# Kernel tuning notes

Hardware: AMD Instinct MI355X
Metric: run time of the kernel (lower is better)

Reference implementation:

```python
import jax, jax.numpy as jnp
import numpy as np

B, M, N, E = 64, 100, 6400, 102400   # graphs, nodes/graph, total nodes, edges
H, D, EMB, IMG, NC = 4, 512, 768, 1024, 2
HD = H * D
EPS = 1e-5


def _bn2(x, g, b, m, v):
    # BatchNorm1d eval mode on [B, C]
    return (x - m) / jnp.sqrt(v + EPS) * g + b


def _bn3(x, g, b, m, v):
    # BatchNorm1d eval mode on [B, C, L] -> channel dim is axis 1 (node index)
    return (x - m[None, :, None]) / jnp.sqrt(v + EPS)[None, :, None] * g[None, :, None] + b[None, :, None]


def _gat(feat, src, dst, W, al, ar, bias):
    # DGL GATConv (eval: feat_drop is identity). feat: [N, F_in]
    h = (feat @ W.T).reshape(-1, H, D)                 # [N, H, D]
    el = (h * al[None]).sum(-1)                         # [N, H]
    er = (h * ar[None]).sum(-1)                         # [N, H]
    e = jax.nn.leaky_relu(el[src] + er[dst], negative_slope=0.2)  # [E, H]
    mx = jax.ops.segment_max(e, dst, num_segments=N)
    a = jnp.exp(e - mx[dst])
    s = jax.ops.segment_sum(a, dst, num_segments=N)
    alpha = a / s[dst]                                  # edge softmax over incoming edges
    out = jax.ops.segment_sum(h[src] * alpha[:, :, None], dst, num_segments=N)  # [N, H, D]
    return out + bias.reshape(1, H, D)


def setup_inputs() -> dict:
    key = jax.random.key(0)
    ks = iter(jax.random.split(key, 80))
    n = lambda *s: jax.random.normal(next(ks), s, dtype=jnp.float32)

    def bn(c):
        return (1.0 + 0.1 * n(c), 0.1 * n(c), 0.1 * n(c),
                0.5 + jax.random.uniform(next(ks), (c,), dtype=jnp.float32))

    s = 0.02
    inp = {}
    inp['img_embedding'] = n(B, IMG)
    inp['func_text_embedding'] = n(B, EMB)
    inp['unix_emb'] = n(N, EMB)
    inp['pos_emb'] = jax.random.uniform(next(ks), (N, 4), dtype=jnp.float32)
    inp['src'] = jax.random.randint(next(ks), (E,), 0, N)
    inp['dst'] = jax.random.randint(next(ks), (E,), 0, N)
    inp['gat1_W'] = n(HD, EMB) * s; inp['gat1_al'] = n(H, D) * 0.1; inp['gat1_ar'] = n(H, D) * 0.1; inp['gat1_b'] = jnp.zeros(HD)
    inp['gat2_W'] = n(HD, HD) * s; inp['gat2_al'] = n(H, D) * 0.1; inp['gat2_ar'] = n(H, D) * 0.1; inp['gat2_b'] = jnp.zeros(HD)
    inp['fc_W'] = n(D, HD) * s; inp['fc_b'] = jnp.zeros(D)
    inp['hidden_W'] = n(8, D, D) * s; inp['hidden_b'] = jnp.zeros((8, D))
    inp['bn_text_g'], inp['bn_text_b'], inp['bn_text_m'], inp['bn_text_v'] = bn(EMB)
    inp['fc_text_W'] = n(D, EMB) * s; inp['fc_text_b'] = jnp.zeros(D)
    inp['swin_g'], inp['swin_b'], inp['swin_m'], inp['swin_v'] = bn(IMG)
    inp['swinfc_W'] = n(D, IMG) * s; inp['swinfc_b'] = jnp.zeros(D)
    inp['bngat_g'], inp['bngat_b'], inp['bngat_m'], inp['bngat_v'] = bn(M)
    inp['fc_gat_W'] = n(480, D) * s; inp['fc_gat_b'] = jnp.zeros(480)
    inp['bnbb_g'], inp['bnbb_b'], inp['bnbb_m'], inp['bnbb_v'] = bn(M)
    inp['fc_bbox_W'] = n(32, 4) * s; inp['fc_bbox_b'] = jnp.zeros(32)
    inp['fbn_g'], inp['fbn_b'], inp['fbn_m'], inp['fbn_v'] = bn(3 * D)
    inp['final_W'] = n(NC, 3 * D) * s; inp['final_b'] = jnp.zeros(NC)
    return inp


def reference(img_embedding, func_text_embedding, unix_emb, pos_emb, src, dst,
              gat1_W, gat1_al, gat1_ar, gat1_b, gat2_W, gat2_al, gat2_ar, gat2_b,
              fc_W, fc_b, hidden_W, hidden_b,
              bn_text_g, bn_text_b, bn_text_m, bn_text_v, fc_text_W, fc_text_b,
              swin_g, swin_b, swin_m, swin_v, swinfc_W, swinfc_b,
              bngat_g, bngat_b, bngat_m, bngat_v, fc_gat_W, fc_gat_b,
              bnbb_g, bnbb_b, bnbb_m, bnbb_v, fc_bbox_W, fc_bbox_b,
              fbn_g, fbn_b, fbn_m, fbn_v, final_W, final_b):
    # image branch
    x = jax.nn.elu(_bn2(img_embedding, swin_g, swin_b, swin_m, swin_v) @ swinfc_W.T + swinfc_b)
    # text branch
    ft = jax.nn.elu(_bn2(func_text_embedding, bn_text_g, bn_text_b, bn_text_m, bn_text_v) @ fc_text_W.T + fc_text_b)
    # graph branch: two stacked GATConv layers (dropout is identity in eval)
    h = _gat(unix_emb, src, dst, gat1_W, gat1_al, gat1_ar, gat1_b).reshape(N, HD)
    h = _gat(h, src, dst, gat2_W, gat2_al, gat2_ar, gat2_b).reshape(N, HD)
    h = jax.nn.elu(h @ fc_W.T + fc_b)
    for i in range(8):
        h = jax.nn.elu(h @ hidden_W[i].T + hidden_b[i])
    # unbatch + pad to max_node=100 -> pure reshape (all graphs have exactly M nodes)
    h_i = h.reshape(B, M, D)
    pos_i = pos_emb.reshape(B, M, 4)
    h_i = jax.nn.elu(_bn3(h_i, bngat_g, bngat_b, bngat_m, bngat_v) @ fc_gat_W.T + fc_gat_b)      # [B, M, 480]
    pos_i = jax.nn.elu(_bn3(pos_i, bnbb_g, bnbb_b, bnbb_m, bnbb_v) @ fc_bbox_W.T + fc_bbox_b)    # [B, M, 32]
    h_feature = jnp.concatenate([h_i, pos_i], axis=2).mean(axis=1)                                # [B, 512]
    all_feats = jnp.concatenate([x, h_feature, ft], axis=1)                                       # [B, 1536]
    return _bn2(all_feats, fbn_g, fbn_b, fbn_m, fbn_v) @ final_W.T + final_b
```

## Files before the change

kernel.cpp:

```cpp
#include <hip/hip_runtime.h>
#include <math.h>

#define Bg   64
#define Mg   100
#define Ng   6400
#define Eg   102400
#define Hh   4
#define Dd   512
#define HDd  2048
#define EMBd 768
#define IMGd 1024
#define EPSc 1e-5f

typedef __bf16 bf16x8 __attribute__((ext_vector_type(8)));
typedef float  f32x4  __attribute__((ext_vector_type(4)));

#define SBAR __builtin_amdgcn_sched_barrier(0)
#define WBAR __builtin_amdgcn_s_barrier()

__device__ __forceinline__ float eluf(float x) { return x > 0.f ? x : expm1f(x); }

__device__ __forceinline__ unsigned short f2bf(float x) {
    unsigned int u = __builtin_bit_cast(unsigned int, x);
    u += 0x7FFFu + ((u >> 16) & 1u);
    return (unsigned short)(u >> 16);
}
__device__ __forceinline__ float bf2f(unsigned short s) {
    return __builtin_bit_cast(float, ((unsigned int)s) << 16);
}

__device__ __forceinline__ void gld16(const void* g, void* l) {
    __builtin_amdgcn_global_load_lds(
        (const __attribute__((address_space(1))) void*)g,
        (__attribute__((address_space(3))) void*)l, 16, 0, 0);
}

__global__ __launch_bounds__(512, 2)
void gemm_bf16_256(const unsigned short* __restrict__ A,
                   const unsigned short* __restrict__ W,
                   const float* __restrict__ bias, void* __restrict__ C,
                   int M, int N, int K, int act, int outbf)
{
    __shared__ __align__(16) unsigned short As[2][256 * 64];
    __shared__ __align__(16) unsigned short Bs[2][256 * 64];

    const int tid  = threadIdx.x;
    const int lane = tid & 63, wid = tid >> 6;
    const int wm = wid >> 2, wn = wid & 3;
    const int bm = blockIdx.y * 256, bn = blockIdx.x * 256;
    const int fl = lane & 15;
    const int fsl = lane >> 4;

    f32x4 acc[8][4] = {};
    bf16x8 a_[4][2];
    bf16x8 b_[2][2][2];

    const int NT = K >> 6;

    const int srow0 = tid >> 3;
    const int scol  = (((tid & 7) ^ ((tid >> 3) & 7)) << 3);
    const unsigned short* pAs = A + (size_t)(bm + srow0) * K + scol;
    const unsigned short* pBs = W + (size_t)(bn + srow0) * K + scol;
    const size_t K64 = (size_t)K * 64, K128 = (size_t)K * 128;

#define STGA(kt, h, d)                                                        \
    do {                                                                      \
        gld16(pAs + (h) * K128 + ((kt) << 6),                                 \
              (char*)As[d] + (h) * 16384 + wid * 1024);                       \
        gld16(pAs + (h) * K128 + K64 + ((kt) << 6),                           \
              (char*)As[d] + (h) * 16384 + 8192 + wid * 1024);                \
    } while (0)
#define STGB(kt, h, d)                                                        \
    do {                                                                      \
        gld16(pBs + (h) * K128 + ((kt) << 6),                                 \
              (char*)Bs[d] + (h) * 16384 + wid * 1024);                       \
        gld16(pBs + (h) * K128 + K64 + ((kt) << 6),                           \
              (char*)Bs[d] + (h) * 16384 + 8192 + wid * 1024);                \
    } while (0)

#define LDA(qm, d)                                                            \
    _Pragma("unroll") for (int i = 0; i < 4; ++i)                             \
    _Pragma("unroll") for (int kk = 0; kk < 2; ++kk) {                        \
        int r_  = wm * 128 + (qm) * 64 + i * 16 + fl;                         \
        int sl_ = ((kk << 2) + fsl) ^ (fl & 7);                               \
        a_[i][kk] = *(const bf16x8*)((const char*)As[d] + r_ * 128 + (sl_ << 4)); \
    }
#define LDB(qn, d)                                                            \
    _Pragma("unroll") for (int j = 0; j < 2; ++j)                             \
    _Pragma("unroll") for (int kk = 0; kk < 2; ++kk) {                        \
        int r_  = wn * 64 + (qn) * 32 + j * 16 + fl;                          \
        int sl_ = ((kk << 2) + fsl) ^ (fl & 7);                               \
        b_[qn][j][kk] = *(const bf16x8*)((const char*)Bs[d] + r_ * 128 + (sl_ << 4)); \
    }
#define PHMM(qm, qn)                                                          \
    do {                                                                      \
        WBAR;                                                                 \
        __builtin_amdgcn_s_setprio(1);                                        \
        _Pragma("unroll") for (int kk = 0; kk < 2; ++kk)                      \
        _Pragma("unroll") for (int i = 0; i < 4; ++i)                         \
        _Pragma("unroll") for (int j = 0; j < 2; ++j)                         \
            acc[(qm) * 4 + i][(qn) * 2 + j] =                                 \
                __builtin_amdgcn_mfma_f32_16x16x32_bf16(                      \
                    a_[i][kk], b_[qn][j][kk],                                 \
                    acc[(qm) * 4 + i][(qn) * 2 + j], 0, 0, 0);                \
        __builtin_amdgcn_s_setprio(0);                                        \
        WBAR;                                                                 \
    } while (0)

    STGB(0, 0, 0); STGB(0, 1, 0);
    STGA(0, 0, 0); STGA(0, 1, 0);
    STGB(1, 0, 1); STGB(1, 1, 1);
    asm volatile("s_waitcnt vmcnt(4)" ::: "memory");
    WBAR;

    for (int j = 0; j < (NT >> 1); ++j) {
        const int O = 2 * j + 1;
        const int g1 = (2 * j + 2 < NT), g2 = (2 * j + 3 < NT);

        LDA(0, 0); LDB(0, 0);
        STGA(O, 0, 1);
        PHMM(0, 0);

        LDB(1, 0);
        STGA(O, 1, 1);
        PHMM(0, 1);

        LDA(1, 0);
        if (g1) STGB(2 * j + 2, 0, 0);
        PHMM(1, 0);

        if (g1) STGB(2 * j + 2, 1, 0);
        if (g1) { asm volatile("s_waitcnt vmcnt(4)" ::: "memory"); }
        else    { asm volatile("s_waitcnt vmcnt(0)" ::: "memory"); }
        PHMM(1, 1);

        LDA(0, 1); LDB(0, 1);
        if (g1) STGA(2 * j + 2, 0, 0);
        PHMM(0, 0);

        LDB(1, 1);
        if (g1) STGA(2 * j + 2, 1, 0);
        PHMM(0, 1);

        LDA(1, 1);
        if (g2) STGB(2 * j + 3, 0, 1);
        PHMM(1, 0);

        if (g2) STGB(2 * j + 3, 1, 1);
        if (g1) { asm volatile("s_waitcnt vmcnt(4)" ::: "memory"); }
        else    { asm volatile("s_waitcnt vmcnt(0)" ::: "memory"); }
        PHMM(1, 1);
    }

#undef STGA
#undef STGB
#undef LDA
#undef LDB
#undef PHMM

    const int crow0 = bm + wm * 128 + ((lane >> 4) << 2);
    const int ccol0 = bn + wn * 64 + fl;
#pragma unroll
    for (int fr = 0; fr < 8; ++fr) {
#pragma unroll
        for (int fc = 0; fc < 4; ++fc) {
            int col = ccol0 + fc * 16;
            float bv = bias ? bias[col] : 0.f;
#pragma unroll
            for (int rr = 0; rr < 4; ++rr) {
                int row = crow0 + fr * 16 + rr;
                float v = acc[fr][fc][rr] + bv;
                if (act) v = eluf(v);
                if (outbf) ((unsigned short*)C)[(size_t)row * N + col] = f2bf(v);
                else       ((float*)C)[(size_t)row * N + col] = v;
            }
        }
    }
}

__global__ __launch_bounds__(256)
void gemm_bf16_t64(const unsigned short* __restrict__ A,
                   const unsigned short* __restrict__ W,
                   const float* __restrict__ bias, void* __restrict__ C,
                   int M, int N, int K, int act, int outbf)
{
    __shared__ __align__(16) unsigned short As[2][64 * 32];
    __shared__ __align__(16) unsigned short Bs[2][64 * 32];
    const int tid  = threadIdx.x;
    const int lane = tid & 63, wid = tid >> 6;
    const int bm = blockIdx.y * 64, bn = blockIdx.x * 64;
    const int wm = (wid >> 1) * 32, wn = (wid & 1) * 32;
    const int lrow = lane >> 2;
    const int lcol = (((lane & 3) ^ ((lane >> 3) & 3)) << 3);

    f32x4 acc[2][2] = {};

    const int ra = wid * 16;
    const unsigned short* gA = A + (size_t)(bm + ra + lrow) * K + lcol;
    int rb = bn + ra + lrow; if (rb >= N) rb = N - 1;
    const unsigned short* gB = W + (size_t)rb * K + lcol;

    const int frow = lane & 15;
    const int qsw = (((lane >> 4) ^ ((frow >> 1) & 3)) << 3);
    const int nt = K >> 5;

#define STAGE64(t, b)                           \
    do {                                        \
        const int k0_ = (t) << 5;               \
        gld16(gA + k0_, &As[b][ra * 32]);       \
        gld16(gB + k0_, &Bs[b][ra * 32]);       \
    } while (0)

    STAGE64(0, 0);
    if (nt > 1) STAGE64(1, 1);

    for (int t = 0; t < nt; ++t) {
        const int bi = t & 1;
        if (t + 1 < nt) { asm volatile("s_waitcnt vmcnt(2)" ::: "memory"); }
        else            { asm volatile("s_waitcnt vmcnt(0)" ::: "memory"); }
        WBAR;

        bf16x8 af0 = *(const bf16x8*)&As[bi][(wm + frow) * 32 + qsw];
        bf16x8 af1 = *(const bf16x8*)&As[bi][(wm + 16 + frow) * 32 + qsw];
        bf16x8 bf0 = *(const bf16x8*)&Bs[bi][(wn + frow) * 32 + qsw];
        bf16x8 bf1 = *(const bf16x8*)&Bs[bi][(wn + 16 + frow) * 32 + qsw];
        acc[0][0] = __builtin_amdgcn_mfma_f32_16x16x32_bf16(af0, bf0, acc[0][0], 0, 0, 0);
        acc[0][1] = __builtin_amdgcn_mfma_f32_16x16x32_bf16(af0, bf1, acc[0][1], 0, 0, 0);
        acc[1][0] = __builtin_amdgcn_mfma_f32_16x16x32_bf16(af1, bf0, acc[1][0], 0, 0, 0);
        acc[1][1] = __builtin_amdgcn_mfma_f32_16x16x32_bf16(af1, bf1, acc[1][1], 0, 0, 0);

        WBAR;
        if (t + 2 < nt) STAGE64(t + 2, bi);
    }
#undef STAGE64

    const int crow0 = bm + wm + ((lane >> 4) << 2);
    const int ccol0 = bn + wn + (lane & 15);
#pragma unroll
    for (int mi = 0; mi < 2; ++mi) {
#pragma unroll
        for (int ni = 0; ni < 2; ++ni) {
            int col = ccol0 + ni * 16;
            if (col >= N) continue;
            float bv = bias ? bias[col] : 0.f;
#pragma unroll
            for (int r = 0; r < 4; ++r) {
                int row = crow0 + mi * 16 + r;
                float v = acc[mi][ni][r] + bv;
                if (act) v = eluf(v);
                if (outbf) ((unsigned short*)C)[(size_t)row * N + col] = f2bf(v);
                else       ((float*)C)[(size_t)row * N + col] = v;
            }
        }
    }
}

__global__ __launch_bounds__(256)
void gemm_nt(const float* __restrict__ A, const float* __restrict__ W,
             const float* __restrict__ bias, float* __restrict__ C,
             int M, int N, int K, int act)
{
    __shared__ float As[16 * 68];
    __shared__ float Ws[16 * 68];
    const int tid = threadIdx.x;
    const int tx = tid & 15, ty = tid >> 4;
    const int bm = blockIdx.y * 64, bn = blockIdx.x * 64;
    const int lrow = tid >> 2;
    const int lk4  = (tid & 3) << 2;
    const int arow = bm + lrow;
    const int wrow = bn + lrow;
    const float* Aptr = A + (size_t)arow * K + lk4;
    const float* Wptr = W + (size_t)wrow * K + lk4;
    float acc[4][4] = {{0.f,0.f,0.f,0.f},{0.f,0.f,0.f,0.f},{0.f,0.f,0.f,0.f},{0.f,0.f,0.f,0.f}};

    for (int k0 = 0; k0 < K; k0 += 16) {
        float4 av = make_float4(0.f,0.f,0.f,0.f);
        float4 wv = make_float4(0.f,0.f,0.f,0.f);
        if (arow < M) av = *(const float4*)(Aptr + k0);
        if (wrow < N) wv = *(const float4*)(Wptr + k0);
        As[(lk4+0)*68 + lrow] = av.x;
        As[(lk4+1)*68 + lrow] = av.y;
        As[(lk4+2)*68 + lrow] = av.z;
        As[(lk4+3)*68 + lrow] = av.w;
        Ws[(lk4+0)*68 + lrow] = wv.x;
        Ws[(lk4+1)*68 + lrow] = wv.y;
        Ws[(lk4+2)*68 + lrow] = wv.z;
        Ws[(lk4+3)*68 + lrow] = wv.w;
        __syncthreads();
#pragma unroll
        for (int kk = 0; kk < 16; ++kk) {
            float4 a = *(const float4*)&As[kk*68 + (ty<<2)];
            float4 w = *(const float4*)&Ws[kk*68 + (tx<<2)];
            acc[0][0] += a.x*w.x; acc[0][1] += a.x*w.y; acc[0][2] += a.x*w.z; acc[0][3] += a.x*w.w;
            acc[1][0] += a.y*w.x; acc[1][1] += a.y*w.y; acc[1][2] += a.y*w.z; acc[1][3] += a.y*w.w;
            acc[2][0] += a.z*w.x; acc[2][1] += a.z*w.y; acc[2][2] += a.z*w.z; acc[2][3] += a.z*w.w;
            acc[3][0] += a.w*w.x; acc[3][1] += a.w*w.y; acc[3][2] += a.w*w.z; acc[3][3] += a.w*w.w;
        }
        __syncthreads();
    }

#pragma unroll
    for (int i = 0; i < 4; ++i) {
        int row = bm + (ty<<2) + i;
        int col = bn + (tx<<2);
        if (row < M && col < N) {
            float4 v;
            v.x = acc[i][0]; v.y = acc[i][1]; v.z = acc[i][2]; v.w = acc[i][3];
            if (bias) { v.x += bias[col]; v.y += bias[col+1]; v.z += bias[col+2]; v.w += bias[col+3]; }
            if (act == 1) { v.x = eluf(v.x); v.y = eluf(v.y); v.z = eluf(v.z); v.w = eluf(v.w); }
            *(float4*)(C + (size_t)row * N + col) = v;
        }
    }
}

struct CvtPack {
    const float* s[6];
    unsigned short* d[6];
    int n4[6];
};

__global__ void cvt_all(CvtPack p, int total4)
{
    int i = blockIdx.x * 256 + threadIdx.x;
    if (i >= total4) return;
#pragma unroll
    for (int k = 0; k < 6; ++k) {
        if (i < p.n4[k]) {
            float4 v = ((const float4*)p.s[k])[i];
            ushort4 o;
            o.x = f2bf(v.x); o.y = f2bf(v.y); o.z = f2bf(v.z); o.w = f2bf(v.w);
            ((ushort4*)p.d[k])[i] = o;
            return;
        }
        i -= p.n4[k];
    }
}

__global__ void bn_col(const float* __restrict__ x, const float* __restrict__ g,
                       const float* __restrict__ b, const float* __restrict__ m,
                       const float* __restrict__ v, float* __restrict__ y,
                       int rows, int cols)
{
    int i = blockIdx.x * 256 + threadIdx.x;
    if (i >= rows * cols) return;
    int c = i % cols;
    float inv = rsqrtf(v[c] + EPSc);
    y[i] = (x[i] - m[c]) * inv * g[c] + b[c];
}

__global__ void bn_node_b4(const ushort4* __restrict__ x, const float* __restrict__ g,
                           const float* __restrict__ b, const float* __restrict__ m,
                           const float* __restrict__ v, ushort4* __restrict__ y,
                           int total4, int Cdim4)
{
    int i = blockIdx.x * 256 + threadIdx.x;
    if (i >= total4) return;
    int n = i / Cdim4;
    int p = n % Mg;
    float sc = rsqrtf(v[p] + EPSc) * g[p];
    float sh = b[p] - m[p] * sc;
    ushort4 xv = x[i];
    ushort4 o;
    o.x = f2bf(bf2f(xv.x) * sc + sh);
    o.y = f2bf(bf2f(xv.y) * sc + sh);
    o.z = f2bf(bf2f(xv.z) * sc + sh);
    o.w = f2bf(bf2f(xv.w) * sc + sh);
    y[i] = o;
}

__global__ void zero_i32(int* __restrict__ p, int n)
{
    int i = blockIdx.x * 256 + threadIdx.x;
    if (i < n) p[i] = 0;
}

__global__ void count_dst(const int* __restrict__ dst, int* __restrict__ counts, int E)
{
    int i = blockIdx.x * 256 + threadIdx.x;
    if (i < E) atomicAdd(&counts[dst[i]], 1);
}

__global__ __launch_bounds__(1024)
void scan_excl(const int* __restrict__ counts, int* __restrict__ offs,
               int* __restrict__ cursor, int n)
{
    __shared__ int sm[1024];
    __shared__ int carry;
    if (threadIdx.x == 0) carry = 0;
    __syncthreads();
    for (int base = 0; base < n; base += 1024) {
        int i = base + (int)threadIdx.x;
        int v = (i < n) ? counts[i] : 0;
        sm[threadIdx.x] = v;
        __syncthreads();
        for (int o = 1; o < 1024; o <<= 1) {
            int t = (threadIdx.x >= (unsigned)o) ? sm[threadIdx.x - o] : 0;
            __syncthreads();
            sm[threadIdx.x] += t;
            __syncthreads();
        }
        int incl = sm[threadIdx.x];
        int myc = carry;
        if (i < n) {
            int ex = myc + incl - v;
            offs[i] = ex;
            cursor[i] = ex;
        }
        __syncthreads();
        if (threadIdx.x == 1023) carry = myc + sm[1023];
        __syncthreads();
    }
    if (threadIdx.x == 0) offs[n] = carry;
}

__global__ void scatter_edges(const int* __restrict__ dst, int* __restrict__ cursor,
                              int* __restrict__ eid, int E)
{
    int i = blockIdx.x * 256 + threadIdx.x;
    if (i < E) {
        int p = atomicAdd(&cursor[dst[i]], 1);
        eid[p] = i;
    }
}

__global__ __launch_bounds__(256)
void elr_kernel(const unsigned short* __restrict__ Hm, const float* __restrict__ al,
                const float* __restrict__ ar, float* __restrict__ el,
                float* __restrict__ er)
{
    int wid = threadIdx.x >> 6, lane = threadIdx.x & 63;
    int g = (blockIdx.x << 2) + wid;
    int n = g >> 2, h = g & 3;
    const unsigned short* hp = Hm + ((size_t)n << 11) + (h << 9) + (lane << 3);
    const float* alp = al + (h << 9) + (lane << 3);
    const float* arp = ar + (h << 9) + (lane << 3);
    ushort4 x0 = *(const ushort4*)hp;
    ushort4 x1 = *(const ushort4*)(hp + 4);
    float4 l0 = *(const float4*)alp, l1 = *(const float4*)(alp + 4);
    float4 r0 = *(const float4*)arp, r1 = *(const float4*)(arp + 4);
    float a0 = bf2f(x0.x), a1 = bf2f(x0.y), a2 = bf2f(x0.z), a3 = bf2f(x0.w);
    float a4 = bf2f(x1.x), a5 = bf2f(x1.y), a6 = bf2f(x1.z), a7 = bf2f(x1.w);
    float se = a0*l0.x + a1*l0.y + a2*l0.z + a3*l0.w + a4*l1.x + a5*l1.y + a6*l1.z + a7*l1.w;
    float sr = a0*r0.x + a1*r0.y + a2*r0.z + a3*r0.w + a4*r1.x + a5*r1.y + a6*r1.z + a7*r1.w;
#pragma unroll
    for (int o = 32; o > 0; o >>= 1) {
        se += __shfl_down(se, o, 64);
        sr += __shfl_down(sr, o, 64);
    }
    if (lane == 0) { el[g] = se; er[g] = sr; }
}

__global__ __launch_bounds__(256)
void gat_agg(const unsigned short* __restrict__ Hm, const float* __restrict__ el,
             const float* __restrict__ er, const int* __restrict__ src,
             const int* __restrict__ offs, const int* __restrict__ eid,
             const float* __restrict__ bias, unsigned short* __restrict__ out)
{
    int n = blockIdx.x;
    int tid = threadIdx.x;
    int beg = offs[n], end = offs[n + 1];
    int deg = end - beg;
    const int b0 = tid << 2;
    const int b1 = 1024 + (tid << 2);
    const int h0 = tid >> 7;
    const int h1 = h0 + 2;

    if (deg == 0) {
#pragma unroll
        for (int j = 0; j < 4; ++j) {
            out[((size_t)n << 11) + b0 + j] = f2bf(bias[b0 + j]);
            out[((size_t)n << 11) + b1 + j] = f2bf(bias[b1 + j]);
        }
        return;
    }

    __shared__ float m_sh[4], s_sh[4], al_sh[4];
    __shared__ int   src_sh[128];
    __shared__ float logit_sh[512];
    __shared__ float w_sh[512];

    if (tid < 4) { m_sh[tid] = -INFINITY; s_sh[tid] = 0.f; }
    float acc[8] = {0.f,0.f,0.f,0.f,0.f,0.f,0.f,0.f};
    __syncthreads();

    for (int c0 = 0; c0 < deg; c0 += 128) {
        int cnt = min(128, deg - c0);
        for (int i = tid; i < cnt; i += 256) src_sh[i] = src[eid[beg + c0 + i]];
        __syncthreads();
        for (int idx = tid; idx < (cnt << 2); idx += 256) {
            int i = idx >> 2, h = idx & 3;
            float x = el[(src_sh[i] << 2) + h] + er[(n << 2) + h];
            logit_sh[idx] = x > 0.f ? x : 0.2f * x;
        }
        __syncthreads();
        if (tid < 4) {
            float cm = -INFINITY;
            for (int i = 0; i < cnt; ++i) cm = fmaxf(cm, logit_sh[(i << 2) + tid]);
            float mn = fmaxf(m_sh[tid], cm);
            al_sh[tid] = expf(m_sh[tid] - mn);
            m_sh[tid] = mn;
        }
        __syncthreads();
        for (int idx = tid; idx < (cnt << 2); idx += 256)
            w_sh[idx] = expf(logit_sh[idx] - m_sh[idx & 3]);
        __syncthreads();
        if (tid < 4) {
            float cs = 0.f;
            for (int i = 0; i < cnt; ++i) cs += w_sh[(i << 2) + tid];
            s_sh[tid] = s_sh[tid] * al_sh[tid] + cs;
        }
        float r0 = al_sh[h0], r1 = al_sh[h1];
        acc[0] *= r0; acc[1] *= r0; acc[2] *= r0; acc[3] *= r0;
        acc[4] *= r1; acc[5] *= r1; acc[6] *= r1; acc[7] *= r1;
        for (int i = 0; i < cnt; ++i) {
            const unsigned short* hp = Hm + ((size_t)src_sh[i] << 11);
            ushort4 a = *(const ushort4*)(hp + b0);
            ushort4 b = *(const ushort4*)(hp + b1);
            float w0 = w_sh[(i << 2) + h0], w1 = w_sh[(i << 2) + h1];
            acc[0] += w0 * bf2f(a.x); acc[1] += w0 * bf2f(a.y);
            acc[2] += w0 * bf2f(a.z); acc[3] += w0 * bf2f(a.w);
            acc[4] += w1 * bf2f(b.x); acc[5] += w1 * bf2f(b.y);
            acc[6] += w1 * bf2f(b.z); acc[7] += w1 * bf2f(b.w);
        }
        __syncthreads();
    }

    float is0 = 1.f / s_sh[h0], is1 = 1.f / s_sh[h1];
#pragma unroll
    for (int j = 0; j < 4; ++j) {
        out[((size_t)n << 11) + b0 + j] = f2bf(acc[j] * is0 + bias[b0 + j]);
        out[((size_t)n << 11) + b1 + j] = f2bf(acc[4 + j] * is1 + bias[b1 + j]);
    }
}

__global__ void mean_kernel(const float* __restrict__ hg, const float* __restrict__ pos,
                            const float* __restrict__ bg, const float* __restrict__ bb_,
                            const float* __restrict__ bm_, const float* __restrict__ bv_,
                            const float* __restrict__ W, const float* __restrict__ bias,
                            float* __restrict__ hf)
{
    int i = blockIdx.x * 256 + threadIdx.x;
    if (i >= Bg * Dd) return;
    int bb = i >> 9, c = i & 511;
    float s = 0.f;
    if (c < 480) {
        const float* p = hg + (size_t)bb * Mg * 480 + c;
        for (int mm = 0; mm < Mg; ++mm) s += p[mm * 480];
    } else {
        int o = c - 480;
        float w0 = W[(o << 2) + 0], w1 = W[(o << 2) + 1];
        float w2 = W[(o << 2) + 2], w3 = W[(o << 2) + 3];
        float bo = bias[o];
        const float* pp = pos + (size_t)bb * Mg * 4;
        for (int mm = 0; mm < Mg; ++mm) {
            float sc = rsqrtf(bv_[mm] + EPSc) * bg[mm];
            float sh = bb_[mm] - bm_[mm] * sc;
            float a = bo + (pp[mm*4+0]*sc+sh)*w0 + (pp[mm*4+1]*sc+sh)*w1
                         + (pp[mm*4+2]*sc+sh)*w2 + (pp[mm*4+3]*sc+sh)*w3;
            s += eluf(a);
        }
    }
    hf[i] = s * 0.01f;
}

__global__ __launch_bounds__(256)
void final_kernel(const float* __restrict__ x, const float* __restrict__ hf,
                  const float* __restrict__ ft, const float* __restrict__ g,
                  const float* __restrict__ b, const float* __restrict__ m,
                  const float* __restrict__ v, const float* __restrict__ W,
                  const float* __restrict__ bias, float* __restrict__ out)
{
    int bb = blockIdx.x;
    int tid = threadIdx.x;
    float a0 = 0.f, a1 = 0.f;
    for (int c = tid; c < 1536; c += 256) {
        float xv = (c < 512) ? x[bb * 512 + c]
                 : (c < 1024) ? hf[bb * 512 + (c - 512)]
                              : ft[bb * 512 + (c - 1024)];
        float z = (xv - m[c]) * rsqrtf(v[c] + EPSc) * g[c] + b[c];
        a0 += z * W[c];
        a1 += z * W[1536 + c];
    }
    __shared__ float r0[256], r1[256];
    r0[tid] = a0; r1[tid] = a1;
    __syncthreads();
    for (int o = 128; o > 0; o >>= 1) {
        if (tid < o) { r0[tid] += r0[tid + o]; r1[tid] += r1[tid + o]; }
        __syncthreads();
    }
    if (tid == 0) {
        out[bb * 2 + 0] = r0[0] + bias[0];
        out[bb * 2 + 1] = r1[0] + bias[1];
    }
}

extern "C" void kernel_launch(void* const* d_in, const int* in_sizes, int n_in,
                              void* d_out, int out_size, void* d_ws, size_t ws_size,
                              hipStream_t stream)
{
    (void)in_sizes; (void)n_in; (void)out_size; (void)ws_size;

    const float* img   = (const float*)d_in[0];
    const float* ftxt  = (const float*)d_in[1];
    const float* unixe = (const float*)d_in[2];
    const float* pos   = (const float*)d_in[3];
    const int*   src   = (const int*)  d_in[4];
    const int*   dst   = (const int*)  d_in[5];
    const float* g1W   = (const float*)d_in[6];
    const float* g1al  = (const float*)d_in[7];
    const float* g1ar  = (const float*)d_in[8];
    const float* g1b   = (const float*)d_in[9];
    const float* g2W   = (const float*)d_in[10];
    const float* g2al  = (const float*)d_in[11];
    const float* g2ar  = (const float*)d_in[12];
    const float* g2b   = (const float*)d_in[13];
    const float* fcW   = (const float*)d_in[14];
    const float* fcb   = (const float*)d_in[15];
    const float* hidW  = (const float*)d_in[16];
    const float* hidb  = (const float*)d_in[17];
    const float* btg   = (const float*)d_in[18];
    const float* btb   = (const float*)d_in[19];
    const float* btm   = (const float*)d_in[20];
    const float* btv   = (const float*)d_in[21];
    const float* ftW   = (const float*)d_in[22];
    const float* ftbi  = (const float*)d_in[23];
    const float* swg   = (const float*)d_in[24];
    const float* swb   = (const float*)d_in[25];
    const float* swm   = (const float*)d_in[26];
    const float* swv   = (const float*)d_in[27];
    const float* swW   = (const float*)d_in[28];
    const float* swbi  = (const float*)d_in[29];
    const float* bgg   = (const float*)d_in[30];
    const float* bgb   = (const float*)d_in[31];
    const float* bgm   = (const float*)d_in[32];
    const float* bgv   = (const float*)d_in[33];
    const float* fgW   = (const float*)d_in[34];
    const float* fgb   = (const float*)d_in[35];
    const float* bbgp  = (const float*)d_in[36];
    const float* bbbp  = (const float*)d_in[37];
    const float* bbmp  = (const float*)d_in[38];
    const float* bbvp  = (const float*)d_in[39];
    const float* fbW   = (const float*)d_in[40];
    const float* fbb   = (const float*)d_in[41];
    const float* fng   = (const float*)d_in[42];
    const float* fnb   = (const float*)d_in[43];
    const float* fnm   = (const float*)d_in[44];
    const float* fnv   = (const float*)d_in[45];
    const float* fiW   = (const float*)d_in[46];
    const float* fib   = (const float*)d_in[47];
    float* out = (float*)d_out;

    char* p = (char*)d_ws;
    unsigned short* fA  = (unsigned short*)p; p += (size_t)Ng * HDd * 2;
    unsigned short* fB  = (unsigned short*)p; p += (size_t)Ng * HDd * 2;
    unsigned short* fC  = (unsigned short*)p; p += (size_t)Ng * Dd * 2;
    unsigned short* fD  = (unsigned short*)p; p += (size_t)Ng * Dd * 2;
    float*          fE  = (float*)p;          p += (size_t)Ng * 480 * 4;
    float*          el  = (float*)p;          p += (size_t)Ng * Hh * 4;
    float*          er  = (float*)p;          p += (size_t)Ng * Hh * 4;
    float*          xb  = (float*)p;          p += (size_t)Bg * Dd * 4;
    float*          ftb = (float*)p;          p += (size_t)Bg * Dd * 4;
    float*          hf  = (float*)p;          p += (size_t)Bg * Dd * 4;
    float*          ti  = (float*)p;          p += (size_t)Bg * IMGd * 4;
    float*          tt  = (float*)p;          p += (size_t)Bg * EMBd * 4;
    unsigned short* ubf = (unsigned short*)p; p += (size_t)Ng * EMBd * 2;
    unsigned short* wg1 = (unsigned short*)p; p += (size_t)HDd * EMBd * 2;
    unsigned short* wg2 = (unsigned short*)p; p += (size_t)HDd * HDd * 2;
    unsigned short* wfc = (unsigned short*)p; p += (size_t)Dd * HDd * 2;
    unsigned short* whid= (unsigned short*)p; p += (size_t)8 * Dd * Dd * 2;
    unsigned short* wfg = (unsigned short*)p; p += (size_t)480 * Dd * 2;
    int* counts = (int*)p; p += (size_t)Ng * 4;
    int* offs   = (int*)p; p += (size_t)(Ng + 1) * 4 + 12;
    int* cursor = (int*)p; p += (size_t)Ng * 4;
    int* eid    = (int*)p; p += (size_t)Eg * 4;

    CvtPack cp;
    cp.s[0] = unixe; cp.d[0] = ubf;  cp.n4[0] = Ng * EMBd / 4;
    cp.s[1] = g1W;   cp.d[1] = wg1;  cp.n4[1] = HDd * EMBd / 4;
    cp.s[2] = g2W;   cp.d[2] = wg2;  cp.n4[2] = HDd * HDd / 4;
    cp.s[3] = fcW;   cp.d[3] = wfc;  cp.n4[3] = Dd * HDd / 4;
    cp.s[4] = hidW;  cp.d[4] = whid; cp.n4[4] = 8 * Dd * Dd / 4;
    cp.s[5] = fgW;   cp.d[5] = wfg;  cp.n4[5] = 480 * Dd / 4;
    int total4 = cp.n4[0] + cp.n4[1] + cp.n4[2] + cp.n4[3] + cp.n4[4] + cp.n4[5];
    cvt_all<<<(total4 + 255)/256, 256, 0, stream>>>(cp, total4);

    bn_col<<<(Bg*IMGd + 255)/256, 256, 0, stream>>>(img, swg, swb, swm, swv, ti, Bg, IMGd);
    gemm_nt<<<dim3(8, 1), 256, 0, stream>>>(ti, swW, swbi, xb, Bg, Dd, IMGd, 1);
    bn_col<<<(Bg*EMBd + 255)/256, 256, 0, stream>>>(ftxt, btg, btb, btm, btv, tt, Bg, EMBd);
    gemm_nt<<<dim3(8, 1), 256, 0, stream>>>(tt, ftW, ftbi, ftb, Bg, Dd, EMBd, 1);

    zero_i32<<<(Ng + 255)/256, 256, 0, stream>>>(counts, Ng);
    count_dst<<<(Eg + 255)/256, 256, 0, stream>>>(dst, counts, Eg);
    scan_excl<<<1, 1024, 0, stream>>>(counts, offs, cursor, Ng);
    scatter_edges<<<(Eg + 255)/256, 256, 0, stream>>>(dst, cursor, eid, Eg);

    gemm_bf16_256<<<dim3(HDd/256, Ng/256), 512, 0, stream>>>(ubf, wg1, nullptr, fA, Ng, HDd, EMBd, 0, 1);
    elr_kernel<<<Ng, 256, 0, stream>>>(fA, g1al, g1ar, el, er);
    gat_agg<<<Ng, 256, 0, stream>>>(fA, el, er, src, offs, eid, g1b, fB);

    gemm_bf16_256<<<dim3(HDd/256, Ng/256), 512, 0, stream>>>(fB, wg2, nullptr, fA, Ng, HDd, HDd, 0, 1);
    elr_kernel<<<Ng, 256, 0, stream>>>(fA, g2al, g2ar, el, er);
    gat_agg<<<Ng, 256, 0, stream>>>(fA, el, er, src, offs, eid, g2b, fB);

    gemm_bf16_t64<<<dim3(Dd/64, Ng/64), 256, 0, stream>>>(fB, wfc, fcb, fC, Ng, Dd, HDd, 1, 1);

    unsigned short* cur = fC; unsigned short* nxt = fD;
    for (int i = 0; i < 8; ++i) {
        gemm_bf16_t64<<<dim3(Dd/64, Ng/64), 256, 0, stream>>>(
            cur, whid + (size_t)i * Dd * Dd, hidb + (size_t)i * Dd, nxt, Ng, Dd, Dd, 1, 1);
        unsigned short* t = cur; cur = nxt; nxt = t;
    }

    bn_node_b4<<<(Ng*Dd/4 + 255)/256, 256, 0, stream>>>(
        (const ushort4*)cur, bgg, bgb, bgm, bgv, (ushort4*)nxt, Ng*Dd/4, Dd/4);
    gemm_bf16_t64<<<dim3(8, Ng/64), 256, 0, stream>>>(nxt, wfg, fgb, fE, Ng, 480, Dd, 1, 0);

    mean_kernel<<<(Bg*Dd + 255)/256, 256, 0, stream>>>(fE, pos, bbgp, bbbp, bbmp, bbvp, fbW, fbb, hf);

    final_kernel<<<Bg, 256, 0, stream>>>(xb, hf, ftb, fng, fnb, fnm, fnv, fiW, fib, out);
}
```

Baseline: 790.1 us.

## Fuse GAT attention logits, batchnorms into GEMM epilogues and prologues

```diff
diff --git a/kernel.cpp b/kernel.cpp
--- a/kernel.cpp
+++ b/kernel.cpp
@@ -39,7 +39,9 @@
 void gemm_bf16_256(const unsigned short* __restrict__ A,
                    const unsigned short* __restrict__ W,
                    const float* __restrict__ bias, void* __restrict__ C,
-                   int M, int N, int K, int act, int outbf)
+                   int M, int N, int K, int act, int outbf,
+                   const float* __restrict__ al, const float* __restrict__ ar,
+                   float* __restrict__ elp, float* __restrict__ erp)
 {
     __shared__ __align__(16) unsigned short As[2][256 * 64];
     __shared__ __align__(16) unsigned short Bs[2][256 * 64];
@@ -160,6 +162,17 @@
 
     const int crow0 = bm + wm * 128 + ((lane >> 4) << 2);
     const int ccol0 = bn + wn * 64 + fl;
+    const int head  = bn >> 9;
+
+    float alv[4], arv[4];
+    if (elp) {
+#pragma unroll
+        for (int fc = 0; fc < 4; ++fc) {
+            alv[fc] = al[ccol0 + fc * 16];
+            arv[fc] = ar[ccol0 + fc * 16];
+        }
+    }
+
 #pragma unroll
     for (int fr = 0; fr < 8; ++fr) {
 #pragma unroll
@@ -175,6 +188,28 @@
                 else       ((float*)C)[(size_t)row * N + col] = v;
             }
         }
+        if (elp) {
+#pragma unroll
+            for (int rr = 0; rr < 4; ++rr) {
+                float se = 0.f, sr = 0.f;
+#pragma unroll
+                for (int fc = 0; fc < 4; ++fc) {
+                    float v = bf2f(f2bf(acc[fr][fc][rr]));
+                    se += v * alv[fc];
+                    sr += v * arv[fc];
+                }
+#pragma unroll
+                for (int m = 1; m < 16; m <<= 1) {
+                    se += __shfl_xor(se, m, 64);
+                    sr += __shfl_xor(sr, m, 64);
+                }
+                if ((lane & 15) == 0) {
+                    int row = crow0 + fr * 16 + rr;
+                    atomicAdd(&elp[(row << 2) | head], se);
+                    atomicAdd(&erp[(row << 2) | head], sr);
+                }
+            }
+        }
     }
 }
 
@@ -182,7 +217,9 @@
 void gemm_bf16_t64(const unsigned short* __restrict__ A,
                    const unsigned short* __restrict__ W,
                    const float* __restrict__ bias, void* __restrict__ C,
-                   int M, int N, int K, int act, int outbf)
+                   int M, int N, int K, int act, int outbf,
+                   const float* __restrict__ rg, const float* __restrict__ rb,
+                   const float* __restrict__ rm, const float* __restrict__ rv)
 {
     __shared__ __align__(16) unsigned short As[2][64 * 32];
     __shared__ __align__(16) unsigned short Bs[2][64 * 32];
@@ -197,8 +234,8 @@
 
     const int ra = wid * 16;
     const unsigned short* gA = A + (size_t)(bm + ra + lrow) * K + lcol;
-    int rb = bn + ra + lrow; if (rb >= N) rb = N - 1;
-    const unsigned short* gB = W + (size_t)rb * K + lcol;
+    int rbn = bn + ra + lrow; if (rbn >= N) rbn = N - 1;
+    const unsigned short* gB = W + (size_t)rbn * K + lcol;
 
     const int frow = lane & 15;
     const int qsw = (((lane >> 4) ^ ((frow >> 1) & 3)) << 3);
@@ -248,6 +285,11 @@
                 int row = crow0 + mi * 16 + r;
                 float v = acc[mi][ni][r] + bv;
                 if (act) v = eluf(v);
+                if (rg) {
+                    int prow = row % Mg;
+                    float sc = rsqrtf(rv[prow] + EPSc) * rg[prow];
+                    v = v * sc + (rb[prow] - rm[prow] * sc);
+                }
                 if (outbf) ((unsigned short*)C)[(size_t)row * N + col] = f2bf(v);
                 else       ((float*)C)[(size_t)row * N + col] = v;
             }
@@ -258,7 +300,9 @@
 __global__ __launch_bounds__(256)
 void gemm_nt(const float* __restrict__ A, const float* __restrict__ W,
              const float* __restrict__ bias, float* __restrict__ C,
-             int M, int N, int K, int act)
+             int M, int N, int K, int act,
+             const float* __restrict__ cg, const float* __restrict__ cb,
+             const float* __restrict__ cm, const float* __restrict__ cv)
 {
     __shared__ float As[16 * 68];
     __shared__ float Ws[16 * 68];
@@ -276,7 +320,16 @@
     for (int k0 = 0; k0 < K; k0 += 16) {
         float4 av = make_float4(0.f,0.f,0.f,0.f);
         float4 wv = make_float4(0.f,0.f,0.f,0.f);
-        if (arow < M) av = *(const float4*)(Aptr + k0);
+        if (arow < M) {
+            av = *(const float4*)(Aptr + k0);
+            if (cg) {
+                int c = k0 + lk4;
+                av.x = (av.x - cm[c+0]) * rsqrtf(cv[c+0] + EPSc) * cg[c+0] + cb[c+0];
+                av.y = (av.y - cm[c+1]) * rsqrtf(cv[c+1] + EPSc) * cg[c+1] + cb[c+1];
+                av.z = (av.z - cm[c+2]) * rsqrtf(cv[c+2] + EPSc) * cg[c+2] + cb[c+2];
+                av.w = (av.w - cm[c+3]) * rsqrtf(cv[c+3] + EPSc) * cg[c+3] + cb[c+3];
+            }
+        }
         if (wrow < N) wv = *(const float4*)(Wptr + k0);
         As[(lk4+0)*68 + lrow] = av.x;
         As[(lk4+1)*68 + lrow] = av.y;
@@ -336,38 +389,6 @@
     }
 }
 
-__global__ void bn_col(const float* __restrict__ x, const float* __restrict__ g,
-                       const float* __restrict__ b, const float* __restrict__ m,
-                       const float* __restrict__ v, float* __restrict__ y,
-                       int rows, int cols)
-{
-    int i = blockIdx.x * 256 + threadIdx.x;
-    if (i >= rows * cols) return;
-    int c = i % cols;
-    float inv = rsqrtf(v[c] + EPSc);
-    y[i] = (x[i] - m[c]) * inv * g[c] + b[c];
-}
-
-__global__ void bn_node_b4(const ushort4* __restrict__ x, const float* __restrict__ g,
-                           const float* __restrict__ b, const float* __restrict__ m,
-                           const float* __restrict__ v, ushort4* __restrict__ y,
-                           int total4, int Cdim4)
-{
-    int i = blockIdx.x * 256 + threadIdx.x;
-    if (i >= total4) return;
-    int n = i / Cdim4;
-    int p = n % Mg;
-    float sc = rsqrtf(v[p] + EPSc) * g[p];
-    float sh = b[p] - m[p] * sc;
-    ushort4 xv = x[i];
-    ushort4 o;
-    o.x = f2bf(bf2f(xv.x) * sc + sh);
-    o.y = f2bf(bf2f(xv.y) * sc + sh);
-    o.z = f2bf(bf2f(xv.z) * sc + sh);
-    o.w = f2bf(bf2f(xv.w) * sc + sh);
-    y[i] = o;
-}
-
 __global__ void zero_i32(int* __restrict__ p, int n)
 {
     int i = blockIdx.x * 256 + threadIdx.x;
@@ -421,33 +442,6 @@
         int p = atomicAdd(&cursor[dst[i]], 1);
         eid[p] = i;
     }
-}
-
-__global__ __launch_bounds__(256)
-void elr_kernel(const unsigned short* __restrict__ Hm, const float* __restrict__ al,
-                const float* __restrict__ ar, float* __restrict__ el,
-                float* __restrict__ er)
-{
-    int wid = threadIdx.x >> 6, lane = threadIdx.x & 63;
-    int g = (blockIdx.x << 2) + wid;
-    int n = g >> 2, h = g & 3;
-    const unsigned short* hp = Hm + ((size_t)n << 11) + (h << 9) + (lane << 3);
-    const float* alp = al + (h << 9) + (lane << 3);
-    const float* arp = ar + (h << 9) + (lane << 3);
-    ushort4 x0 = *(const ushort4*)hp;
-    ushort4 x1 = *(const ushort4*)(hp + 4);
-    float4 l0 = *(const float4*)alp, l1 = *(const float4*)(alp + 4);
-    float4 r0 = *(const float4*)arp, r1 = *(const float4*)(arp + 4);
-    float a0 = bf2f(x0.x), a1 = bf2f(x0.y), a2 = bf2f(x0.z), a3 = bf2f(x0.w);
-    float a4 = bf2f(x1.x), a5 = bf2f(x1.y), a6 = bf2f(x1.z), a7 = bf2f(x1.w);
-    float se = a0*l0.x + a1*l0.y + a2*l0.z + a3*l0.w + a4*l1.x + a5*l1.y + a6*l1.z + a7*l1.w;
-    float sr = a0*r0.x + a1*r0.y + a2*r0.z + a3*r0.w + a4*r1.x + a5*r1.y + a6*r1.z + a7*r1.w;
-#pragma unroll
-    for (int o = 32; o > 0; o >>= 1) {
-        se += __shfl_down(se, o, 64);
-        sr += __shfl_down(sr, o, 64);
-    }
-    if (lane == 0) { el[g] = se; er[g] = sr; }
 }
 
 __global__ __launch_bounds__(256)
@@ -684,36 +678,43 @@
     int total4 = cp.n4[0] + cp.n4[1] + cp.n4[2] + cp.n4[3] + cp.n4[4] + cp.n4[5];
     cvt_all<<<(total4 + 255)/256, 256, 0, stream>>>(cp, total4);
 
-    bn_col<<<(Bg*IMGd + 255)/256, 256, 0, stream>>>(img, swg, swb, swm, swv, ti, Bg, IMGd);
-    gemm_nt<<<dim3(8, 1), 256, 0, stream>>>(ti, swW, swbi, xb, Bg, Dd, IMGd, 1);
-    bn_col<<<(Bg*EMBd + 255)/256, 256, 0, stream>>>(ftxt, btg, btb, btm, btv, tt, Bg, EMBd);
-    gemm_nt<<<dim3(8, 1), 256, 0, stream>>>(tt, ftW, ftbi, ftb, Bg, Dd, EMBd, 1);
+    gemm_nt<<<dim3(8, 1), 256, 0, stream>>>(img, swW, swbi, xb, Bg, Dd, IMGd, 1,
+                                            swg, swb, swm, swv);
+    gemm_nt<<<dim3(8, 1), 256, 0, stream>>>(ftxt, ftW, ftbi, ftb, Bg, Dd, EMBd, 1,
+                                            btg, btb, btm, btv);
 
     zero_i32<<<(Ng + 255)/256, 256, 0, stream>>>(counts, Ng);
     count_dst<<<(Eg + 255)/256, 256, 0, stream>>>(dst, counts, Eg);
     scan_excl<<<1, 1024, 0, stream>>>(counts, offs, cursor, Ng);
     scatter_edges<<<(Eg + 255)/256, 256, 0, stream>>>(dst, cursor, eid, Eg);
 
-    gemm_bf16_256<<<dim3(HDd/256, Ng/256), 512, 0, stream>>>(ubf, wg1, nullptr, fA, Ng, HDd, EMBd, 0, 1);
-    elr_kernel<<<Ng, 256, 0, stream>>>(fA, g1al, g1ar, el, er);
+    zero_i32<<<(2*Ng*Hh + 255)/256, 256, 0, stream>>>((int*)el, 2*Ng*Hh);
+    gemm_bf16_256<<<dim3(HDd/256, Ng/256), 512, 0, stream>>>(
+        ubf, wg1, nullptr, fA, Ng, HDd, EMBd, 0, 1, g1al, g1ar, el, er);
     gat_agg<<<Ng, 256, 0, stream>>>(fA, el, er, src, offs, eid, g1b, fB);
 
-    gemm_bf16_256<<<dim3(HDd/256, Ng/256), 512, 0, stream>>>(fB, wg2, nullptr, fA, Ng, HDd, HDd, 0, 1);
-    elr_kernel<<<Ng, 256, 0, stream>>>(fA, g2al, g2ar, el, er);
+    zero_i32<<<(2*Ng*Hh + 255)/256, 256, 0, stream>>>((int*)el, 2*Ng*Hh);
+    gemm_bf16_256<<<dim3(HDd/256, Ng/256), 512, 0, stream>>>(
+        fB, wg2, nullptr, fA, Ng, HDd, HDd, 0, 1, g2al, g2ar, el, er);
     gat_agg<<<Ng, 256, 0, stream>>>(fA, el, er, src, offs, eid, g2b, fB);
 
-    gemm_bf16_t64<<<dim3(Dd/64, Ng/64), 256, 0, stream>>>(fB, wfc, fcb, fC, Ng, Dd, HDd, 1, 1);
+    gemm_bf16_t64<<<dim3(Dd/64, Ng/64), 256, 0, stream>>>(
+        fB, wfc, fcb, fC, Ng, Dd, HDd, 1, 1, nullptr, nullptr, nullptr, nullptr);
 
     unsigned short* cur = fC; unsigned short* nxt = fD;
     for (int i = 0; i < 8; ++i) {
+        const float* rg = (i == 7) ? bgg : nullptr;
+        const float* rb = (i == 7) ? bgb : nullptr;
+        const float* rm = (i == 7) ? bgm : nullptr;
+        const float* rv = (i == 7) ? bgv : nullptr;
         gemm_bf16_t64<<<dim3(Dd/64, Ng/64), 256, 0, stream>>>(
-            cur, whid + (size_t)i * Dd * Dd, hidb + (size_t)i * Dd, nxt, Ng, Dd, Dd, 1, 1);
+            cur, whid + (size_t)i * Dd * Dd, hidb + (size_t)i * Dd, nxt, Ng, Dd, Dd, 1, 1,
+            rg, rb, rm, rv);
         unsigned short* t = cur; cur = nxt; nxt = t;
     }
 
-    bn_node_b4<<<(Ng*Dd/4 + 255)/256, 256, 0, stream>>>(
-        (const ushort4*)cur, bgg, bgb, bgm, bgv, (ushort4*)nxt, Ng*Dd/4, Dd/4);
-    gemm_bf16_t64<<<dim3(8, Ng/64), 256, 0, stream>>>(nxt, wfg, fgb, fE, Ng, 480, Dd, 1, 0);
+    gemm_bf16_t64<<<dim3(8, Ng/64), 256, 0, stream>>>(
+        cur, wfg, fgb, fE, Ng, 480, Dd, 1, 0, nullptr, nullptr, nullptr, nullptr);
 
     mean_kernel<<<(Bg*Dd + 255)/256, 256, 0, stream>>>(fE, pos, bbgp, bbbp, bbmp, bbvp, fbW, fbb, hf);
 
```

Measured after the change: 849.7 us. 7.5% more time.
